# Optimization experiments

Measured on AMD Instinct MI355X. Metric: run time of the kernel, lower is better.

## Reference

```python
import jax, jax.numpy as jnp
import numpy as np

B, S, H, L, NH, T, V = 16, 512, 768, 6, 12, 32, 10000


def setup_inputs() -> dict:
    key = jax.random.key(0)
    ks = jax.random.split(key, 16)
    p = lambda i, shape: jax.random.normal(ks[i], shape, jnp.float32) * 0.02
    return {
        "input_ids": jax.random.randint(ks[0], (B, S), 0, V),
        "labels": jax.random.randint(ks[1], (B, S), 0, T),
        "if_crf": 1,
        "emb": p(2, (V, H)),
        "attn_in_w": p(3, (L, 3 * H, H)), "attn_in_b": p(4, (L, 3 * H)),
        "attn_out_w": p(5, (L, H, H)), "attn_out_b": p(6, (L, H)),
        "ln1_g": jnp.ones((L, H), jnp.float32), "ln1_b": jnp.zeros((L, H), jnp.float32),
        "ln2_g": jnp.ones((L, H), jnp.float32), "ln2_b": jnp.zeros((L, H), jnp.float32),
        "ffn_w1": p(7, (L, H, H)), "ffn_b1": p(8, (L, H)),
        "ffn_w2": p(9, (L, H, H)), "ffn_b2": p(10, (L, H)),
        "head_w": p(11, (T, H)), "head_b": p(12, (T,)),
        "crf_start": p(13, (T,)), "crf_end": p(14, (T,)), "crf_trans": p(15, (T, T)),
    }


def _layer_norm(x, g, b, eps=1e-5):
    m = x.mean(-1, keepdims=True)
    v = ((x - m) ** 2).mean(-1, keepdims=True)
    return (x - m) * jax.lax.rsqrt(v + eps) * g + b


def _encoder(x, params):
    # PyTorch post-norm TransformerEncoderLayer, batch_first, relu, dropout=0 (eval)
    def layer(x, p):
        in_w, in_b, out_w, out_b, g1, b1, g2, b2, w1, bb1, w2, bb2 = p
        Bq, Sq, Hq = x.shape
        dh = Hq // NH
        qkv = x @ in_w.T + in_b                       # [B,S,3H]
        q, k, v = jnp.split(qkv, 3, axis=-1)
        q = q.reshape(Bq, Sq, NH, dh).transpose(0, 2, 1, 3)
        k = k.reshape(Bq, Sq, NH, dh).transpose(0, 2, 1, 3)
        v = v.reshape(Bq, Sq, NH, dh).transpose(0, 2, 1, 3)
        scale = 1.0 / np.sqrt(dh).astype(np.float32).item()
        a = jax.nn.softmax(jnp.einsum('bhqd,bhkd->bhqk', q, k) * scale, axis=-1)
        o = jnp.einsum('bhqk,bhkd->bhqd', a, v).transpose(0, 2, 1, 3).reshape(Bq, Sq, Hq)
        o = o @ out_w.T + out_b
        x = _layer_norm(x + o, g1, b1)
        ff = jax.nn.relu(x @ w1.T + bb1) @ w2.T + bb2
        x = _layer_norm(x + ff, g2, b2)
        return x, None
    x, _ = jax.lax.scan(layer, x, params)
    return x


def _crf_llh(emis, tags, start, end, trans):
    # torchcrf log-likelihood, no mask, reduction='sum'
    Bq = emis.shape[0]
    emit = jnp.take_along_axis(emis, tags[:, :, None], axis=2)[:, :, 0].sum(1)   # [B]
    tr = trans[tags[:, :-1], tags[:, 1:]].sum(1)                                 # [B]
    num = start[tags[:, 0]] + emit + tr + end[tags[:, -1]]
    # partition via forward algorithm (scan over time)
    def step(score, e_t):  # score [B,T], e_t [B,T]
        ns = jax.nn.logsumexp(score[:, :, None] + trans[None], axis=1) + e_t
        return ns, None
    score0 = start[None] + emis[:, 0]
    scoreN, _ = jax.lax.scan(step, score0, jnp.swapaxes(emis, 0, 1)[1:])
    logZ = jax.nn.logsumexp(scoreN + end[None], axis=1)
    return (num - logZ).sum()


def _viterbi(emis, start, end, trans):
    score0 = start[None] + emis[:, 0]
    def step(score, e_t):
        cand = score[:, :, None] + trans[None]   # [B,T,T]
        return cand.max(1) + e_t, cand.argmax(1)
    scoreN, hist = jax.lax.scan(step, score0, jnp.swapaxes(emis, 0, 1)[1:])  # hist [S-1,B,T]
    last = (scoreN + end[None]).argmax(1)  # [B]
    def back(tag, h_t):
        prev = jnp.take_along_axis(h_t, tag[:, None], axis=1)[:, 0]
        return prev, prev
    _, prevs = jax.lax.scan(back, last, hist, reverse=True)  # prevs[i] = tag at pos i
    return jnp.concatenate([prevs.T, last[:, None]], axis=1)  # [B,S]


def reference(input_ids, labels, if_crf, emb, attn_in_w, attn_in_b, attn_out_w, attn_out_b,
              ln1_g, ln1_b, ln2_g, ln2_b, ffn_w1, ffn_b1, ffn_w2, ffn_b2,
              head_w, head_b, crf_start, crf_end, crf_trans):
    x = emb[input_ids]
    params = (attn_in_w, attn_in_b, attn_out_w, attn_out_b, ln1_g, ln1_b, ln2_g, ln2_b,
              ffn_w1, ffn_b1, ffn_w2, ffn_b2)
    logits = _encoder(x, params)            # [B,S,H]
    emis = logits @ head_w.T + head_b       # [B,S,T]
    if if_crf:
        llh = _crf_llh(emis, labels, crf_start, crf_end, crf_trans)
        tags = _viterbi(emis, crf_start, crf_end, crf_trans)
        return logits, -llh / 10000.0, tags
    else:
        return logits, emis, jnp.argmax(emis, axis=-1)
```

## Files before the change

kernel.cpp:

```cpp
#include <hip/hip_runtime.h>

#define MTOK 8192
#define HD   768
#define H3   2304
#define NL   6
#define TT   32

typedef __attribute__((ext_vector_type(4))) float f32x4;
typedef __attribute__((ext_vector_type(8))) short v8bf;
typedef __attribute__((ext_vector_type(4))) unsigned short us4;
typedef __attribute__((ext_vector_type(8))) unsigned short us8;

__device__ __forceinline__ unsigned short bf16rne(float v) {
    unsigned int u = __float_as_uint(v);
    u += 0x7FFFu + ((u >> 16) & 1u);
    return (unsigned short)(u >> 16);
}
__device__ __forceinline__ float bf2f(unsigned short h) {
    return __uint_as_float(((unsigned int)h) << 16);
}
__device__ __forceinline__ unsigned int split_pack(float v) {
    unsigned short h = bf16rne(v);
    unsigned short m = bf16rne(v - bf2f(h));
    return (unsigned int)h | ((unsigned int)m << 16);
}

__device__ __forceinline__ void gload16(const unsigned short* g, unsigned short* l) {
    __builtin_amdgcn_global_load_lds(
        (const __attribute__((address_space(1))) unsigned int*)g,
        (__attribute__((address_space(3))) unsigned int*)l, 16, 0, 0);
}

__global__ __launch_bounds__(256)
void wsplit4_kernel(const float* __restrict__ inw, const float* __restrict__ outw,
                    const float* __restrict__ w1, const float* __restrict__ w2,
                    unsigned short* __restrict__ wih, unsigned short* __restrict__ wim,
                    unsigned short* __restrict__ woh, unsigned short* __restrict__ wom,
                    unsigned short* __restrict__ w1h, unsigned short* __restrict__ w1m,
                    unsigned short* __restrict__ w2h, unsigned short* __restrict__ w2m)
{
    int i = blockIdx.x * 256 + threadIdx.x;
    const float* src; unsigned short* dh; unsigned short* dm; int off;
    if (i < 442368)      { src = inw;  dh = wih; dm = wim; off = i; }
    else if (i < 589824) { src = outw; dh = woh; dm = wom; off = i - 442368; }
    else if (i < 737280) { src = w1;   dh = w1h; dm = w1m; off = i - 589824; }
    else                 { src = w2;   dh = w2h; dm = w2m; off = i - 737280; }
    float4 v = reinterpret_cast<const float4*>(src)[off];
    us4 hv, mv; unsigned int p;
    p = split_pack(v.x); hv[0] = (unsigned short)p; mv[0] = (unsigned short)(p >> 16);
    p = split_pack(v.y); hv[1] = (unsigned short)p; mv[1] = (unsigned short)(p >> 16);
    p = split_pack(v.z); hv[2] = (unsigned short)p; mv[2] = (unsigned short)(p >> 16);
    p = split_pack(v.w); hv[3] = (unsigned short)p; mv[3] = (unsigned short)(p >> 16);
    reinterpret_cast<us4*>(dh)[off] = hv;
    reinterpret_cast<us4*>(dm)[off] = mv;
}

template<bool RELU, bool SPLITOUT>
__global__ __launch_bounds__(256)
void gemm_pair_kernel(const unsigned short* __restrict__ Ahg, const unsigned short* __restrict__ Amg,
                      const unsigned short* __restrict__ Bhg, const unsigned short* __restrict__ Bmg,
                      const float* __restrict__ bias, float* __restrict__ Cf,
                      unsigned short* __restrict__ Ch, unsigned short* __restrict__ Cm, int N)
{
    __shared__ unsigned short lds[4][128 * 64];
    const int tid = threadIdx.x;
    const int lane = tid & 63, wave = tid >> 6;
    const int wm = wave >> 1, wn = wave & 1;
    const int nbx = gridDim.x;
    const int total = nbx * gridDim.y;
    const int flat = blockIdx.y * nbx + blockIdx.x;
    const int sw = (flat & 7) * (total >> 3) + (flat >> 3);
    const int bn = sw % nbx, bm = sw / nbx;
    const int g = lane >> 4, lr = lane & 15;

    const int srow = lane >> 3;
    const int schunk = ((lane & 7) ^ srow) * 8;
    const size_t aoff = ((size_t)(bm * 128 + wave * 32 + srow)) * HD + schunk;
    const size_t boff = ((size_t)(bn * 128 + wave * 32 + srow)) * HD + schunk;

    f32x4 acc[4][4] = {};

    for (int kt = 0; kt < 12; ++kt) {
        __syncthreads();
        const int k64 = kt * 64;
        #pragma unroll
        for (int i = 0; i < 4; ++i) {
            const size_t ra = aoff + (size_t)i * 8 * HD + k64;
            const size_t rb = boff + (size_t)i * 8 * HD + k64;
            unsigned short* lb = (unsigned short*)&lds[0][(wave * 32 + i * 8) * 64];
            gload16(Ahg + ra, lb);
            gload16(Amg + ra, lb + 8192);
            gload16(Bhg + rb, lb + 16384);
            gload16(Bmg + rb, lb + 24576);
        }
        __syncthreads();
        #pragma unroll
        for (int kk = 0; kk < 2; ++kk) {
            v8bf ah[4], am[4], bh[4], bmv[4];
            #pragma unroll
            for (int i = 0; i < 4; ++i) {
                int row = wm * 64 + i * 16 + lr;
                int ub = row * 64 + ((((kk << 2) + g) ^ (row & 7)) << 3);
                ah[i] = *reinterpret_cast<const v8bf*>(&lds[0][ub]);
                am[i] = *reinterpret_cast<const v8bf*>(&lds[1][ub]);
            }
            #pragma unroll
            for (int i = 0; i < 4; ++i) {
                int row = wn * 64 + i * 16 + lr;
                int ub = row * 64 + ((((kk << 2) + g) ^ (row & 7)) << 3);
                bh[i]  = *reinterpret_cast<const v8bf*>(&lds[2][ub]);
                bmv[i] = *reinterpret_cast<const v8bf*>(&lds[3][ub]);
            }
            #pragma unroll
            for (int i = 0; i < 4; ++i)
                #pragma unroll
                for (int j = 0; j < 4; ++j) {
                    acc[i][j] = __builtin_amdgcn_mfma_f32_16x16x32_bf16(ah[i], bh[j],  acc[i][j], 0, 0, 0);
                    acc[i][j] = __builtin_amdgcn_mfma_f32_16x16x32_bf16(ah[i], bmv[j], acc[i][j], 0, 0, 0);
                    acc[i][j] = __builtin_amdgcn_mfma_f32_16x16x32_bf16(am[i], bh[j],  acc[i][j], 0, 0, 0);
                }
        }
    }
    #pragma unroll
    for (int j = 0; j < 4; ++j) {
        int n = bn * 128 + wn * 64 + j * 16 + lr;
        float bv = bias[n];
        #pragma unroll
        for (int i = 0; i < 4; ++i) {
            int mr = bm * 128 + wm * 64 + i * 16 + 4 * g;
            #pragma unroll
            for (int r = 0; r < 4; ++r) {
                float y = acc[i][j][r] + bv;
                if (RELU) y = fmaxf(y, 0.0f);
                size_t idx = (size_t)(mr + r) * N + n;
                if (SPLITOUT) {
                    unsigned int pk = split_pack(y);
                    Ch[idx] = (unsigned short)pk;
                    Cm[idx] = (unsigned short)(pk >> 16);
                } else {
                    Cf[idx] = y;
                }
            }
        }
    }
}

__global__ __launch_bounds__(256)
void vtrans_kernel(const unsigned short* __restrict__ qh, const unsigned short* __restrict__ qm,
                   unsigned short* __restrict__ vth, unsigned short* __restrict__ vtm)
{
    __shared__ unsigned short Th[4096], Tm[4096];
    const int kt = blockIdx.x, bh = blockIdx.y;
    const int b = bh / 12, h = bh % 12;
    const int tid = threadIdx.x;
    #pragma unroll
    for (int is = 0; is < 2; ++is) {
        int c = is * 256 + tid;
        int r = c >> 3, dc = c & 7;
        size_t src = ((size_t)b * 512 + kt * 64 + r) * H3 + 1536 + h * 64 + dc * 8;
        int swz = (dc ^ (r & 7) ^ (r >> 3)) * 8;
        *reinterpret_cast<us8*>(&Th[r * 64 + swz]) = *reinterpret_cast<const us8*>(&qh[src]);
        *reinterpret_cast<us8*>(&Tm[r * 64 + swz]) = *reinterpret_cast<const us8*>(&qm[src]);
    }
    __syncthreads();
    #pragma unroll
    for (int is = 0; is < 2; ++is) {
        int c = is * 256 + tid;
        int d = c >> 3, rg = c & 7;
        us8 vh, vm;
        #pragma unroll
        for (int e = 0; e < 8; ++e) {
            int r = rg * 8 + e;
            int addr = r * 64 + (((d >> 3) ^ (r & 7) ^ (r >> 3)) * 8) + (d & 7);
            vh[e] = Th[addr]; vm[e] = Tm[addr];
        }
        size_t dst = ((size_t)bh * 64 + d) * 512 + kt * 64 + rg * 8;
        *reinterpret_cast<us8*>(&vth[dst]) = vh;
        *reinterpret_cast<us8*>(&vtm[dst]) = vm;
    }
}

__global__ __launch_bounds__(256, 2)
void attn_kernel(const unsigned short* __restrict__ qh, const unsigned short* __restrict__ qm,
                 const unsigned short* __restrict__ vth, const unsigned short* __restrict__ vtm,
                 unsigned short* __restrict__ ohp, unsigned short* __restrict__ omp)
{
    __shared__ unsigned short Kh[4096], Km[4096], Vh[4096], Vm[4096];
    __shared__ unsigned short Ph[4][1024], Pm[4][1024];
    const int qhalf = blockIdx.x;
    const int bh = blockIdx.y;
    const int b = bh / 12, h = bh % 12;
    const int tid = threadIdx.x, lane = tid & 63, wave = tid >> 6;
    const int g = lane >> 4, lr = lane & 15;
    const size_t rowbase = (size_t)b * 512;
    const int qbase = qhalf * 256 + wave * 64;

    v8bf aqh[4][2], aqm[4][2];
    #pragma unroll
    for (int i = 0; i < 4; ++i)
        #pragma unroll
        for (int kk = 0; kk < 2; ++kk) {
            size_t a = (rowbase + qbase + i * 16 + lr) * H3 + h * 64 + (kk * 4 + g) * 8;
            aqh[i][kk] = *reinterpret_cast<const v8bf*>(&qh[a]);
            aqm[i][kk] = *reinterpret_cast<const v8bf*>(&qm[a]);
        }

    float m_run[4][4], l_run[4][4];
    f32x4 O[4][4];
    #pragma unroll
    for (int i = 0; i < 4; ++i)
        #pragma unroll
        for (int r = 0; r < 4; ++r) {
            m_run[i][r] = -__builtin_inff(); l_run[i][r] = 0.0f;
            O[i][r] = (f32x4){0.0f, 0.0f, 0.0f, 0.0f};
        }

    const int srow = lane >> 3;
    const int schunk = ((lane & 7) ^ srow) * 8;

    for (int kt = 0; kt < 8; ++kt) {
        __syncthreads();
        #pragma unroll
        for (int is = 0; is < 2; ++is) {
            int rowg = is * 32 + wave * 8;
            size_t ksrc = (rowbase + kt * 64 + rowg + srow) * H3 + 768 + h * 64 + schunk;
            size_t vsrc = ((size_t)bh * 64 + rowg + srow) * 512 + kt * 64 + schunk;
            gload16(qh + ksrc, &Kh[rowg * 64]);
            gload16(qm + ksrc, &Km[rowg * 64]);
            gload16(vth + vsrc, &Vh[rowg * 64]);
            gload16(vtm + vsrc, &Vm[rowg * 64]);
        }
        __syncthreads();

        #pragma unroll
        for (int i = 0; i < 4; ++i) {
            f32x4 s[4] = {};
            #pragma unroll
            for (int kk = 0; kk < 2; ++kk) {
                #pragma unroll
                for (int j = 0; j < 4; ++j) {
                    int krow = j * 16 + lr;
                    int uk = krow * 64 + (((kk * 4 + g) ^ (krow & 7)) * 8);
                    v8bf bkh = *reinterpret_cast<const v8bf*>(&Kh[uk]);
                    v8bf bkm = *reinterpret_cast<const v8bf*>(&Km[uk]);
                    s[j] = __builtin_amdgcn_mfma_f32_16x16x32_bf16(aqh[i][kk], bkh, s[j], 0, 0, 0);
                    s[j] = __builtin_amdgcn_mfma_f32_16x16x32_bf16(aqh[i][kk], bkm, s[j], 0, 0, 0);
                    s[j] = __builtin_amdgcn_mfma_f32_16x16x32_bf16(aqm[i][kk], bkh, s[j], 0, 0, 0);
                }
            }
            float mnew[4], alpha[4], rsum[4];
            #pragma unroll
            for (int rr = 0; rr < 4; ++rr) {
                float t = fmaxf(fmaxf(s[0][rr], s[1][rr]), fmaxf(s[2][rr], s[3][rr])) * 0.125f;
                #pragma unroll
                for (int off = 1; off < 16; off <<= 1) t = fmaxf(t, __shfl_xor(t, off));
                mnew[rr] = fmaxf(m_run[i][rr], t);
                alpha[rr] = __expf(m_run[i][rr] - mnew[rr]);
                m_run[i][rr] = mnew[rr];
                rsum[rr] = 0.0f;
            }
            #pragma unroll
            for (int j = 0; j < 4; ++j) {
                #pragma unroll
                for (int rr = 0; rr < 4; ++rr) {
                    float p = __expf(s[j][rr] * 0.125f - mnew[rr]);
                    rsum[rr] += p;
                    int prow = 4 * g + rr;
                    int ub = prow * 64 + ((((j * 2 + (lr >> 3)) ^ (prow & 7)) << 3) | (lr & 7));
                    unsigned int pk = split_pack(p);
                    Ph[wave][ub] = (unsigned short)pk; Pm[wave][ub] = (unsigned short)(pk >> 16);
                }
            }
            #pragma unroll
            for (int rr = 0; rr < 4; ++rr) {
                float t = rsum[rr];
                #pragma unroll
                for (int off = 1; off < 16; off <<= 1) t += __shfl_xor(t, off);
                l_run[i][rr] = l_run[i][rr] * alpha[rr] + t;
                O[i][0][rr] *= alpha[rr]; O[i][1][rr] *= alpha[rr];
                O[i][2][rr] *= alpha[rr]; O[i][3][rr] *= alpha[rr];
            }
            #pragma unroll
            for (int kk = 0; kk < 2; ++kk) {
                int up = lr * 64 + (((kk * 4 + g) ^ (lr & 7)) * 8);
                v8bf aph = *reinterpret_cast<const v8bf*>(&Ph[wave][up]);
                v8bf apm = *reinterpret_cast<const v8bf*>(&Pm[wave][up]);
                #pragma unroll
                for (int j = 0; j < 4; ++j) {
                    int vrow = j * 16 + lr;
                    int uv = vrow * 64 + (((kk * 4 + g) ^ (vrow & 7)) * 8);
                    v8bf bvh = *reinterpret_cast<const v8bf*>(&Vh[uv]);
                    v8bf bvm = *reinterpret_cast<const v8bf*>(&Vm[uv]);
                    O[i][j] = __builtin_amdgcn_mfma_f32_16x16x32_bf16(aph, bvh, O[i][j], 0, 0, 0);
                    O[i][j] = __builtin_amdgcn_mfma_f32_16x16x32_bf16(aph, bvm, O[i][j], 0, 0, 0);
                    O[i][j] = __builtin_amdgcn_mfma_f32_16x16x32_bf16(apm, bvh, O[i][j], 0, 0, 0);
                }
            }
        }
    }
    #pragma unroll
    for (int i = 0; i < 4; ++i)
        #pragma unroll
        for (int j = 0; j < 4; ++j) {
            int d = j * 16 + lr;
            #pragma unroll
            for (int rr = 0; rr < 4; ++rr) {
                size_t tok = rowbase + qbase + i * 16 + 4 * g + rr;
                unsigned int pk = split_pack(O[i][j][rr] / l_run[i][rr]);
                ohp[tok * HD + h * 64 + d] = (unsigned short)pk;
                omp[tok * HD + h * 64 + d] = (unsigned short)(pk >> 16);
            }
        }
}

__global__ __launch_bounds__(256)
void ln_residual_kernel(unsigned short* __restrict__ xh, unsigned short* __restrict__ xm,
                        const float* __restrict__ t,
                        const float* __restrict__ gamma, const float* __restrict__ beta)
{
    int tok = blockIdx.x * 4 + (threadIdx.x >> 6);
    int lane = threadIdx.x & 63;
    size_t base = (size_t)tok * HD + lane * 12;
    int cb = lane * 12;
    us4 h4[3], m4[3]; f32x4 t4[3];
    #pragma unroll
    for (int q = 0; q < 3; ++q) {
        h4[q] = *reinterpret_cast<const us4*>(&xh[base + q * 4]);
        m4[q] = *reinterpret_cast<const us4*>(&xm[base + q * 4]);
        t4[q] = *reinterpret_cast<const f32x4*>(&t[base + q * 4]);
    }
    float v[12];
    float s = 0.0f;
    #pragma unroll
    for (int k = 0; k < 12; ++k) {
        v[k] = bf2f(h4[k >> 2][k & 3]) + bf2f(m4[k >> 2][k & 3]) + t4[k >> 2][k & 3];
        s += v[k];
    }
    #pragma unroll
    for (int off = 32; off; off >>= 1) s += __shfl_xor(s, off);
    float mean = s * (1.0f / 768.0f);
    float vs = 0.0f;
    #pragma unroll
    for (int k = 0; k < 12; ++k) { float d = v[k] - mean; vs += d * d; }
    #pragma unroll
    for (int off = 32; off; off >>= 1) vs += __shfl_xor(vs, off);
    float rstd = rsqrtf(vs * (1.0f / 768.0f) + 1e-5f);
    f32x4 ga[3], be[3];
    #pragma unroll
    for (int q = 0; q < 3; ++q) {
        ga[q] = *reinterpret_cast<const f32x4*>(&gamma[cb + q * 4]);
        be[q] = *reinterpret_cast<const f32x4*>(&beta[cb + q * 4]);
    }
    us4 oh[3], om[3];
    #pragma unroll
    for (int k = 0; k < 12; ++k) {
        float y = (v[k] - mean) * rstd * ga[k >> 2][k & 3] + be[k >> 2][k & 3];
        unsigned int pk = split_pack(y);
        oh[k >> 2][k & 3] = (unsigned short)pk;
        om[k >> 2][k & 3] = (unsigned short)(pk >> 16);
    }
    #pragma unroll
    for (int q = 0; q < 3; ++q) {
        *reinterpret_cast<us4*>(&xh[base + q * 4]) = oh[q];
        *reinterpret_cast<us4*>(&xm[base + q * 4]) = om[q];
    }
}

__global__ __launch_bounds__(256)
void embed_kernel(const int* __restrict__ ids, const float* __restrict__ emb,
                  unsigned short* __restrict__ xh, unsigned short* __restrict__ xm)
{
    int f4 = blockIdx.x * 256 + threadIdx.x;
    int tok = f4 / 192, c = f4 % 192;
    float4 v = *reinterpret_cast<const float4*>(emb + (size_t)ids[tok] * HD + c * 4);
    us4 hv, mv; unsigned int p;
    p = split_pack(v.x); hv[0] = (unsigned short)p; mv[0] = (unsigned short)(p >> 16);
    p = split_pack(v.y); hv[1] = (unsigned short)p; mv[1] = (unsigned short)(p >> 16);
    p = split_pack(v.z); hv[2] = (unsigned short)p; mv[2] = (unsigned short)(p >> 16);
    p = split_pack(v.w); hv[3] = (unsigned short)p; mv[3] = (unsigned short)(p >> 16);
    *reinterpret_cast<us4*>(&xh[(size_t)tok * HD + c * 4]) = hv;
    *reinterpret_cast<us4*>(&xm[(size_t)tok * HD + c * 4]) = mv;
}

__global__ __launch_bounds__(256)
void out_logits_kernel(const unsigned short* __restrict__ xh, const unsigned short* __restrict__ xm,
                       float* __restrict__ out)
{
    int i = blockIdx.x * 256 + threadIdx.x;
    us4 hv = reinterpret_cast<const us4*>(xh)[i];
    us4 mv = reinterpret_cast<const us4*>(xm)[i];
    float4 o;
    o.x = bf2f(hv[0]) + bf2f(mv[0]);
    o.y = bf2f(hv[1]) + bf2f(mv[1]);
    o.z = bf2f(hv[2]) + bf2f(mv[2]);
    o.w = bf2f(hv[3]) + bf2f(mv[3]);
    reinterpret_cast<float4*>(out)[i] = o;
}

__global__ __launch_bounds__(256)
void emis_kernel(const unsigned short* __restrict__ xh, const unsigned short* __restrict__ xm,
                 const float* __restrict__ hw, const float* __restrict__ hb,
                 float* __restrict__ emis)
{
    int tok = blockIdx.x * 4 + (threadIdx.x >> 6);
    int lane = threadIdx.x & 63;
    size_t base = (size_t)tok * HD + lane * 12;
    int cb = lane * 12;
    us4 h4[3], m4[3];
    #pragma unroll
    for (int q = 0; q < 3; ++q) {
        h4[q] = *reinterpret_cast<const us4*>(&xh[base + q * 4]);
        m4[q] = *reinterpret_cast<const us4*>(&xm[base + q * 4]);
    }
    float xv[12];
    #pragma unroll
    for (int k = 0; k < 12; ++k)
        xv[k] = bf2f(h4[k >> 2][k & 3]) + bf2f(m4[k >> 2][k & 3]);
    for (int t = 0; t < TT; ++t) {
        f32x4 w4[3];
        #pragma unroll
        for (int q = 0; q < 3; ++q)
            w4[q] = *reinterpret_cast<const f32x4*>(&hw[t * HD + cb + q * 4]);
        float a = 0.0f;
        #pragma unroll
        for (int k = 0; k < 12; ++k) a += xv[k] * w4[k >> 2][k & 3];
        #pragma unroll
        for (int off = 32; off; off >>= 1) a += __shfl_xor(a, off);
        if (lane == 0) emis[(size_t)tok * TT + t] = a + hb[t];
    }
}

__global__ void crf_num_kernel(const float* __restrict__ emis, const int* __restrict__ labels,
                               const float* __restrict__ start, const float* __restrict__ end,
                               const float* __restrict__ trans, float* __restrict__ num)
{
    int b = blockIdx.x, lane = threadIdx.x;
    float a = 0.0f;
    for (int s = lane; s < 512; s += 64) {
        int lab = labels[b * 512 + s];
        a += emis[(size_t)(b * 512 + s) * TT + lab];
        if (s > 0) a += trans[labels[b * 512 + s - 1] * TT + lab];
        else a += start[lab];
        if (s == 511) a += end[lab];
    }
    #pragma unroll
    for (int off = 32; off; off >>= 1) a += __shfl_xor(a, off);
    if (lane == 0) num[b] = a;
}

__global__ __launch_bounds__(64)
void crf_path_kernel(const float* __restrict__ emis, const float* __restrict__ start,
                     const float* __restrict__ end, const float* __restrict__ trans,
                     float* __restrict__ logZ, float* __restrict__ out_tags)
{
    const int mode = blockIdx.x >> 4;
    const int b = blockIdx.x & 15;
    const int lane = threadIdx.x;
    const int j = lane & 31;
    __shared__ float xch[32];
    __shared__ unsigned char hist[511][32];
    __shared__ float sval[32];
    __shared__ int path[512];

    const float* eb = emis + (size_t)b * 512 * TT;

    if (mode == 0) {
        if (lane < 32) {
            float Ecol[32];
            #pragma unroll
            for (int ii = 0; ii < 32; ++ii) Ecol[ii] = __expf(trans[ii * TT + j]);
            float cur[8], nxt[8];
            #pragma unroll
            for (int i = 0; i < 8; ++i) cur[i] = eb[(1 + i) * TT + j];
            float sc = start[j] + eb[j];
            for (int base = 1; base < 512; base += 8) {
                #pragma unroll
                for (int i = 0; i < 8; ++i) {
                    int s = base + 8 + i;
                    nxt[i] = eb[(s < 512 ? s : 511) * TT + j];
                }
                #pragma unroll
                for (int i = 0; i < 8; ++i) {
                    if (base + i < 512) {
                        xch[j] = sc;
                        asm volatile("s_waitcnt lgkmcnt(0)" ::: "memory");
                        f32x4 tt[8];
                        #pragma unroll
                        for (int q = 0; q < 8; ++q)
                            tt[q] = *reinterpret_cast<const f32x4*>(&xch[q * 4]);
                        asm volatile("" ::: "memory");
                        float r = tt[0][0];
                        float m[32];
                        #pragma unroll
                        for (int ii = 0; ii < 32; ++ii)
                            m[ii] = __expf(tt[ii >> 2][ii & 3] - r) * Ecol[ii];
                        float s16[16];
                        #pragma unroll
                        for (int q = 0; q < 16; ++q) s16[q] = m[2 * q] + m[2 * q + 1];
                        float s8[8];
                        #pragma unroll
                        for (int q = 0; q < 8; ++q) s8[q] = s16[2 * q] + s16[2 * q + 1];
                        float sA[4];
                        #pragma unroll
                        for (int q = 0; q < 4; ++q) sA[q] = s8[2 * q] + s8[2 * q + 1];
                        float dot = (sA[0] + sA[1]) + (sA[2] + sA[3]);
                        sc = r + __logf(dot) + cur[i];
                    }
                }
                #pragma unroll
                for (int i = 0; i < 8; ++i) cur[i] = nxt[i];
            }
            float v = sc + end[j];
            float mx = v;
            #pragma unroll
            for (int off = 1; off < 32; off <<= 1) mx = fmaxf(mx, __shfl_xor(mx, off));
            float p = __expf(v - mx);
            float sm = p;
            #pragma unroll
            for (int off = 1; off < 32; off <<= 1) sm += __shfl_xor(sm, off);
            if (lane == 0) logZ[b] = mx + __logf(sm);
        }
    } else {
        if (lane < 32) {
            float tcol[32];
            #pragma unroll
            for (int ii = 0; ii < 32; ++ii) tcol[ii] = trans[ii * TT + j];
            float cur[8], nxt[8];
            #pragma unroll
            for (int i = 0; i < 8; ++i) cur[i] = eb[(1 + i) * TT + j];
            float sc = start[j] + eb[j];
            for (int base = 1; base < 512; base += 8) {
                #pragma unroll
                for (int i = 0; i < 8; ++i) {
                    int s = base + 8 + i;
                    nxt[i] = eb[(s < 512 ? s : 511) * TT + j];
                }
                #pragma unroll
                for (int i = 0; i < 8; ++i) {
                    if (base + i < 512) {
                        int s = base + i;
                        xch[j] = sc;
                        asm volatile("s_waitcnt lgkmcnt(0)" ::: "memory");
                        f32x4 tt[8];
                        #pragma unroll
                        for (int q = 0; q < 8; ++q)
                            tt[q] = *reinterpret_cast<const f32x4*>(&xch[q * 4]);
                        asm volatile("" ::: "memory");
                        float c[32];
                        #pragma unroll
                        for (int ii = 0; ii < 32; ++ii)
                            c[ii] = tt[ii >> 2][ii & 3] + tcol[ii];
                        float v1[16]; int a1[16];
                        #pragma unroll
                        for (int q = 0; q < 16; ++q) {
                            bool ge = c[2 * q] >= c[2 * q + 1];
                            v1[q] = ge ? c[2 * q] : c[2 * q + 1];
                            a1[q] = ge ? 2 * q : 2 * q + 1;
                        }
                        float v2[8]; int a2[8];
                        #pragma unroll
                        for (int q = 0; q < 8; ++q) {
                            bool ge = v1[2 * q] >= v1[2 * q + 1];
                            v2[q] = ge ? v1[2 * q] : v1[2 * q + 1];
                            a2[q] = ge ? a1[2 * q] : a1[2 * q + 1];
                        }
                        float v3[4]; int a3[4];
                        #pragma unroll
                        for (int q = 0; q < 4; ++q) {
                            bool ge = v2[2 * q] >= v2[2 * q + 1];
                            v3[q] = ge ? v2[2 * q] : v2[2 * q + 1];
                            a3[q] = ge ? a2[2 * q] : a2[2 * q + 1];
                        }
                        float v4[2]; int a4[2];
                        #pragma unroll
                        for (int q = 0; q < 2; ++q) {
                            bool ge = v3[2 * q] >= v3[2 * q + 1];
                            v4[q] = ge ? v3[2 * q] : v3[2 * q + 1];
                            a4[q] = ge ? a3[2 * q] : a3[2 * q + 1];
                        }
                        bool ge = v4[0] >= v4[1];
                        float best = ge ? v4[0] : v4[1];
                        int arg = ge ? a4[0] : a4[1];
                        hist[s - 1][j] = (unsigned char)arg;
                        sc = best + cur[i];
                    }
                }
                #pragma unroll
                for (int i = 0; i < 8; ++i) cur[i] = nxt[i];
            }
            sval[j] = sc + end[j];
        }
        __syncthreads();
        if (lane == 0) {
            float best = sval[0]; int arg = 0;
            for (int i = 1; i < TT; ++i)
                if (sval[i] > best) { best = sval[i]; arg = i; }
            int t = arg; path[511] = t;
            for (int s = 510; s >= 0; --s) { t = hist[s][t]; path[s] = t; }
        }
        __syncthreads();
        for (int s = lane; s < 512; s += 64)
            out_tags[(size_t)b * 512 + s] = (float)path[s];
    }
}

__global__ void crf_loss_kernel(const float* __restrict__ num, const float* __restrict__ logZ,
                                float* __restrict__ out)
{
    if (threadIdx.x == 0) {
        float s = 0.0f;
        for (int b = 0; b < 16; ++b) s += num[b] - logZ[b];
        out[0] = -s / 10000.0f;
    }
}

extern "C" void kernel_launch(void* const* d_in, const int* in_sizes, int n_in,
                              void* d_out, int out_size, void* d_ws, size_t ws_size,
                              hipStream_t stream)
{
    (void)in_sizes; (void)n_in; (void)out_size; (void)ws_size;
    const int*   input_ids = (const int*)d_in[0];
    const int*   labels    = (const int*)d_in[1];
    const float* emb   = (const float*)d_in[3];
    const float* in_w  = (const float*)d_in[4];
    const float* in_b  = (const float*)d_in[5];
    const float* out_w = (const float*)d_in[6];
    const float* out_b = (const float*)d_in[7];
    const float* ln1g  = (const float*)d_in[8];
    const float* ln1b  = (const float*)d_in[9];
    const float* ln2g  = (const float*)d_in[10];
    const float* ln2b  = (const float*)d_in[11];
    const float* w1    = (const float*)d_in[12];
    const float* b1    = (const float*)d_in[13];
    const float* w2    = (const float*)d_in[14];
    const float* b2    = (const float*)d_in[15];
    const float* hw    = (const float*)d_in[16];
    const float* hb    = (const float*)d_in[17];
    const float* cs    = (const float*)d_in[18];
    const float* ce    = (const float*)d_in[19];
    const float* ct    = (const float*)d_in[20];
    float* out = (float*)d_out;

    char* ws = (char*)d_ws;
    unsigned short* xh   = (unsigned short*)(ws);
    unsigned short* xm   = (unsigned short*)(ws + 12582912);
    unsigned short* qkvh = (unsigned short*)(ws + 25165824);
    unsigned short* qkvm = (unsigned short*)(ws + 62914560);
    unsigned short* ohb  = (unsigned short*)(ws + 100663296);
    unsigned short* omb  = (unsigned short*)(ws + 113246208);
    float*          tmp  = (float*)(ws + 125829120);
    unsigned short* vth  = (unsigned short*)(ws + 125829120);
    unsigned short* vtm  = (unsigned short*)(ws + 138412032);
    unsigned short* wih  = (unsigned short*)(ws + 150994944);
    unsigned short* wim  = (unsigned short*)(ws + 154533888);
    unsigned short* woh  = (unsigned short*)(ws + 158072832);
    unsigned short* wom  = (unsigned short*)(ws + 159252480);
    unsigned short* w1h  = (unsigned short*)(ws + 160432128);
    unsigned short* w1m  = (unsigned short*)(ws + 161611776);
    unsigned short* w2h  = (unsigned short*)(ws + 162791424);
    unsigned short* w2m  = (unsigned short*)(ws + 163971072);
    unsigned short* f1h  = qkvh;
    unsigned short* f1m  = qkvm;
    float* emis = (float*)(ws + 100663296);
    float* numb = (float*)(ws + 100663296 + 1048576);
    float* logZ = numb + 16;

    embed_kernel<<<MTOK * 192 / 256, 256, 0, stream>>>(input_ids, emb, xh, xm);

    for (int l = 0; l < NL; ++l) {
        wsplit4_kernel<<<3456, 256, 0, stream>>>(
            in_w + (size_t)l * H3 * HD, out_w + (size_t)l * HD * HD,
            w1 + (size_t)l * HD * HD, w2 + (size_t)l * HD * HD,
            wih, wim, woh, wom, w1h, w1m, w2h, w2m);

        gemm_pair_kernel<false, true><<<dim3(18, 64), 256, 0, stream>>>(
            xh, xm, wih, wim, in_b + (size_t)l * H3, nullptr, qkvh, qkvm, H3);
        vtrans_kernel<<<dim3(8, 192), 256, 0, stream>>>(qkvh, qkvm, vth, vtm);
        attn_kernel<<<dim3(2, 192), 256, 0, stream>>>(qkvh, qkvm, vth, vtm, ohb, omb);
        gemm_pair_kernel<false, false><<<dim3(6, 64), 256, 0, stream>>>(
            ohb, omb, woh, wom, out_b + (size_t)l * HD, tmp, nullptr, nullptr, HD);
        ln_residual_kernel<<<2048, 256, 0, stream>>>(xh, xm, tmp, ln1g + l * HD, ln1b + l * HD);
        gemm_pair_kernel<true, true><<<dim3(6, 64), 256, 0, stream>>>(
            xh, xm, w1h, w1m, b1 + (size_t)l * HD, nullptr, f1h, f1m, HD);
        gemm_pair_kernel<false, false><<<dim3(6, 64), 256, 0, stream>>>(
            f1h, f1m, w2h, w2m, b2 + (size_t)l * HD, tmp, nullptr, nullptr, HD);
        ln_residual_kernel<<<2048, 256, 0, stream>>>(xh, xm, tmp, ln2g + l * HD, ln2b + l * HD);
    }

    out_logits_kernel<<<MTOK * 192 / 256, 256, 0, stream>>>(xh, xm, out);

    emis_kernel<<<2048, 256, 0, stream>>>(xh, xm, hw, hb, emis);
    crf_num_kernel<<<16, 64, 0, stream>>>(emis, labels, cs, ce, ct, numb);
    crf_path_kernel<<<32, 64, 0, stream>>>(emis, cs, ce, ct, logZ, out + 6291457);
    crf_loss_kernel<<<1, 64, 0, stream>>>(numb, logZ, out + 6291456);
}
```

Measured before the change: 2.296 ms.

## Shorten CRF forward and Viterbi serial chains; recompute Viterbi argmax after the scan

The forward (logZ) recurrence now exponentiates each state's score once, relative to a wave-uniform reference taken with readfirstlane, before the exchange. It then forms the sum as an FMA dot product with exp(trans), replacing 32 exps per lane per step. The Viterbi scan carries only the max values on its serial path and stores every step's scores to shared memory. Argmax backpointers are recomputed afterwards in a parallel pass that uses both half-waves. This trims the dependent latency of both 511-step recurrences, at the cost of a 64KB shared-memory score buffer, an extra pass, and possible overflow if per-state scores spread widely.

After: 2.239 ms. 1.03x faster.

```diff
diff --git a/kernel.cpp b/kernel.cpp
--- a/kernel.cpp
+++ b/kernel.cpp
@@ -458,6 +458,7 @@
     const int lane = threadIdx.x;
     const int j = lane & 31;
     __shared__ float xch[32];
+    __shared__ float shist[512 * 32];
     __shared__ unsigned char hist[511][32];
     __shared__ float sval[32];
     __shared__ int path[512];
@@ -473,6 +474,64 @@
             #pragma unroll
             for (int i = 0; i < 8; ++i) cur[i] = eb[(1 + i) * TT + j];
             float sc = start[j] + eb[j];
+            for (int base = 1; base < 512; base += 8) {
+                #pragma unroll
+                for (int i = 0; i < 8; ++i) {
+                    int s = base + 8 + i;
+                    nxt[i] = eb[(s < 512 ? s : 511) * TT + j];
+                }
+                #pragma unroll
+                for (int i = 0; i < 8; ++i) {
+                    if (base + i < 512) {
+                        float r = __uint_as_float(
+                            __builtin_amdgcn_readfirstlane(__float_as_uint(sc)));
+                        float p = __expf(sc - r);
+                        xch[j] = p;
+                        asm volatile("s_waitcnt lgkmcnt(0)" ::: "memory");
+                        f32x4 tt[8];
+                        #pragma unroll
+                        for (int q = 0; q < 8; ++q)
+                            tt[q] = *reinterpret_cast<const f32x4*>(&xch[q * 4]);
+                        asm volatile("" ::: "memory");
+                        float mm[16];
+                        #pragma unroll
+                        for (int q = 0; q < 16; ++q)
+                            mm[q] = fmaf(tt[(2 * q + 1) >> 2][(2 * q + 1) & 3], Ecol[2 * q + 1],
+                                         tt[(2 * q) >> 2][(2 * q) & 3] * Ecol[2 * q]);
+                        float s8[8];
+                        #pragma unroll
+                        for (int q = 0; q < 8; ++q) s8[q] = mm[2 * q] + mm[2 * q + 1];
+                        float s4[4];
+                        #pragma unroll
+                        for (int q = 0; q < 4; ++q) s4[q] = s8[2 * q] + s8[2 * q + 1];
+                        float dot = (s4[0] + s4[1]) + (s4[2] + s4[3]);
+                        sc = r + __logf(dot) + cur[i];
+                    }
+                }
+                #pragma unroll
+                for (int i = 0; i < 8; ++i) cur[i] = nxt[i];
+            }
+            float v = sc + end[j];
+            float mx = v;
+            #pragma unroll
+            for (int off = 1; off < 32; off <<= 1) mx = fmaxf(mx, __shfl_xor(mx, off));
+            float p = __expf(v - mx);
+            float sm = p;
+            #pragma unroll
+            for (int off = 1; off < 32; off <<= 1) sm += __shfl_xor(sm, off);
+            if (lane == 0) logZ[b] = mx + __logf(sm);
+        }
+    } else {
+        float tcol[32];
+        #pragma unroll
+        for (int ii = 0; ii < 32; ++ii) tcol[ii] = trans[ii * TT + j];
+
+        if (lane < 32) {
+            float cur[8], nxt[8];
+            #pragma unroll
+            for (int i = 0; i < 8; ++i) cur[i] = eb[(1 + i) * TT + j];
+            float sc = start[j] + eb[j];
+            shist[0 * 32 + j] = sc;
             for (int base = 1; base < 512; base += 8) {
                 #pragma unroll
                 for (int i = 0; i < 8; ++i) {
@@ -489,100 +548,22 @@
                         for (int q = 0; q < 8; ++q)
                             tt[q] = *reinterpret_cast<const f32x4*>(&xch[q * 4]);
                         asm volatile("" ::: "memory");
-                        float r = tt[0][0];
-                        float m[32];
-                        #pragma unroll
-                        for (int ii = 0; ii < 32; ++ii)
-                            m[ii] = __expf(tt[ii >> 2][ii & 3] - r) * Ecol[ii];
-                        float s16[16];
-                        #pragma unroll
-                        for (int q = 0; q < 16; ++q) s16[q] = m[2 * q] + m[2 * q + 1];
-                        float s8[8];
-                        #pragma unroll
-                        for (int q = 0; q < 8; ++q) s8[q] = s16[2 * q] + s16[2 * q + 1];
-                        float sA[4];
-                        #pragma unroll
-                        for (int q = 0; q < 4; ++q) sA[q] = s8[2 * q] + s8[2 * q + 1];
-                        float dot = (sA[0] + sA[1]) + (sA[2] + sA[3]);
-                        sc = r + __logf(dot) + cur[i];
-                    }
-                }
-                #pragma unroll
-                for (int i = 0; i < 8; ++i) cur[i] = nxt[i];
-            }
-            float v = sc + end[j];
-            float mx = v;
-            #pragma unroll
-            for (int off = 1; off < 32; off <<= 1) mx = fmaxf(mx, __shfl_xor(mx, off));
-            float p = __expf(v - mx);
-            float sm = p;
-            #pragma unroll
-            for (int off = 1; off < 32; off <<= 1) sm += __shfl_xor(sm, off);
-            if (lane == 0) logZ[b] = mx + __logf(sm);
-        }
-    } else {
-        if (lane < 32) {
-            float tcol[32];
-            #pragma unroll
-            for (int ii = 0; ii < 32; ++ii) tcol[ii] = trans[ii * TT + j];
-            float cur[8], nxt[8];
-            #pragma unroll
-            for (int i = 0; i < 8; ++i) cur[i] = eb[(1 + i) * TT + j];
-            float sc = start[j] + eb[j];
-            for (int base = 1; base < 512; base += 8) {
-                #pragma unroll
-                for (int i = 0; i < 8; ++i) {
-                    int s = base + 8 + i;
-                    nxt[i] = eb[(s < 512 ? s : 511) * TT + j];
-                }
-                #pragma unroll
-                for (int i = 0; i < 8; ++i) {
-                    if (base + i < 512) {
-                        int s = base + i;
-                        xch[j] = sc;
-                        asm volatile("s_waitcnt lgkmcnt(0)" ::: "memory");
-                        f32x4 tt[8];
-                        #pragma unroll
-                        for (int q = 0; q < 8; ++q)
-                            tt[q] = *reinterpret_cast<const f32x4*>(&xch[q * 4]);
-                        asm volatile("" ::: "memory");
                         float c[32];
                         #pragma unroll
                         for (int ii = 0; ii < 32; ++ii)
                             c[ii] = tt[ii >> 2][ii & 3] + tcol[ii];
-                        float v1[16]; int a1[16];
-                        #pragma unroll
-                        for (int q = 0; q < 16; ++q) {
-                            bool ge = c[2 * q] >= c[2 * q + 1];
-                            v1[q] = ge ? c[2 * q] : c[2 * q + 1];
-                            a1[q] = ge ? 2 * q : 2 * q + 1;
-                        }
-                        float v2[8]; int a2[8];
-                        #pragma unroll
-                        for (int q = 0; q < 8; ++q) {
-                            bool ge = v1[2 * q] >= v1[2 * q + 1];
-                            v2[q] = ge ? v1[2 * q] : v1[2 * q + 1];
-                            a2[q] = ge ? a1[2 * q] : a1[2 * q + 1];
-                        }
-                        float v3[4]; int a3[4];
-                        #pragma unroll
-                        for (int q = 0; q < 4; ++q) {
-                            bool ge = v2[2 * q] >= v2[2 * q + 1];
-                            v3[q] = ge ? v2[2 * q] : v2[2 * q + 1];
-                            a3[q] = ge ? a2[2 * q] : a2[2 * q + 1];
-                        }
-                        float v4[2]; int a4[2];
-                        #pragma unroll
-                        for (int q = 0; q < 2; ++q) {
-                            bool ge = v3[2 * q] >= v3[2 * q + 1];
-                            v4[q] = ge ? v3[2 * q] : v3[2 * q + 1];
-                            a4[q] = ge ? a3[2 * q] : a3[2 * q + 1];
-                        }
-                        bool ge = v4[0] >= v4[1];
-                        float best = ge ? v4[0] : v4[1];
-                        int arg = ge ? a4[0] : a4[1];
-                        hist[s - 1][j] = (unsigned char)arg;
+                        float v1[16];
+                        #pragma unroll
+                        for (int q = 0; q < 16; ++q) v1[q] = fmaxf(c[2 * q], c[2 * q + 1]);
+                        float v2[8];
+                        #pragma unroll
+                        for (int q = 0; q < 8; ++q) v2[q] = fmaxf(v1[2 * q], v1[2 * q + 1]);
+                        float v3[4];
+                        #pragma unroll
+                        for (int q = 0; q < 4; ++q) v3[q] = fmaxf(v2[2 * q], v2[2 * q + 1]);
+                        float best = fmaxf(fmaxf(v3[0], v3[1]), fmaxf(v3[2], v3[3]));
                         sc = best + cur[i];
+                        shist[(base + i) * 32 + j] = sc;
                     }
                 }
                 #pragma unroll
@@ -591,6 +572,56 @@
             sval[j] = sc + end[j];
         }
         __syncthreads();
+
+        const int h = lane >> 5;
+        for (int it = 0; it < 256; ++it) {
+            int s = 1 + 2 * it + h;
+            if (s < 512) {
+                const float* pr = &shist[(s - 1) * 32];
+                float c[32];
+                #pragma unroll
+                for (int q = 0; q < 8; ++q) {
+                    f32x4 t4 = *reinterpret_cast<const f32x4*>(&pr[q * 4]);
+                    c[q * 4 + 0] = t4[0] + tcol[q * 4 + 0];
+                    c[q * 4 + 1] = t4[1] + tcol[q * 4 + 1];
+                    c[q * 4 + 2] = t4[2] + tcol[q * 4 + 2];
+                    c[q * 4 + 3] = t4[3] + tcol[q * 4 + 3];
+                }
+                float v1[16]; int a1[16];
+                #pragma unroll
+                for (int q = 0; q < 16; ++q) {
+                    bool ge = c[2 * q] >= c[2 * q + 1];
+                    v1[q] = ge ? c[2 * q] : c[2 * q + 1];
+                    a1[q] = ge ? 2 * q : 2 * q + 1;
+                }
+                float v2[8]; int a2[8];
+                #pragma unroll
+                for (int q = 0; q < 8; ++q) {
+                    bool ge = v1[2 * q] >= v1[2 * q + 1];
+                    v2[q] = ge ? v1[2 * q] : v1[2 * q + 1];
+                    a2[q] = ge ? a1[2 * q] : a1[2 * q + 1];
+                }
+                float v3[4]; int a3[4];
+                #pragma unroll
+                for (int q = 0; q < 4; ++q) {
+                    bool ge = v2[2 * q] >= v2[2 * q + 1];
+                    v3[q] = ge ? v2[2 * q] : v2[2 * q + 1];
+                    a3[q] = ge ? a2[2 * q] : a2[2 * q + 1];
+                }
+                float v4[2]; int a4[2];
+                #pragma unroll
+                for (int q = 0; q < 2; ++q) {
+                    bool ge = v3[2 * q] >= v3[2 * q + 1];
+                    v4[q] = ge ? v3[2 * q] : v3[2 * q + 1];
+                    a4[q] = ge ? a3[2 * q] : a3[2 * q + 1];
+                }
+                bool ge = v4[0] >= v4[1];
+                int arg = ge ? a4[0] : a4[1];
+                hist[s - 1][j] = (unsigned char)arg;
+            }
+        }
+        __syncthreads();
+
         if (lane == 0) {
             float best = sval[0]; int arg = 0;
             for (int i = 1; i < TT; ++i)
```
